# Kernel tuning notes

Hardware: AMD Instinct MI355X
Metric: run time of the kernel (lower is better)

Reference implementation:

```python
import jax, jax.numpy as jnp
import numpy as np

B, C, VC, H, W = 4, 256, 128, 64, 64


def setup_inputs() -> dict:
    key = jax.random.key(0)
    kx, kq, kk, kv = jax.random.split(key, 4)
    # Conv2d 1x1 no-bias weights are just [out_channels, in_channels] matrices.
    s = 1.0 / np.sqrt(C)
    return {
        "x": jax.random.normal(kx, (B, C, H, W), dtype=jnp.float32),
        "Wq": jax.random.uniform(kq, (VC, C), minval=-s, maxval=s, dtype=jnp.float32),
        "Wk": jax.random.uniform(kk, (VC, C), minval=-s, maxval=s, dtype=jnp.float32),
        "Wv": jax.random.uniform(kv, (VC, C), minval=-s, maxval=s, dtype=jnp.float32),
    }


def reference(x, Wq, Wk, Wv):
    # 1x1 convs == per-pixel channel GEMMs
    Q = jnp.einsum('bchw,dc->bdhw', x, Wq)  # [B, VC, H, W]
    K = jnp.einsum('bchw,dc->bdhw', x, Wk)
    V = jnp.einsum('bchw,dc->bdhw', x, Wv)
    b, d, h, w = Q.shape
    # affinity over all spatial pairs: [B, H, W, H, W]
    aff = jnp.einsum('bdij,bdkl->bijkl', Q, K).reshape(b, h, w, h * w)
    aff = jax.nn.softmax(aff, axis=3).reshape(b, h, w, h, w)
    # attention-weighted aggregation of values
    out = jnp.einsum('bijkl,bdkl->bdij', aff, V)  # [B, VC, H, W]
    return out
```

## Files before the change

### kernel.cpp

```cpp
#include <hip/hip_runtime.h>
#include <hip/hip_bf16.h>

#define B_ 4
#define C_ 256
#define D_ 128
#define N_ 4096

typedef float f32x4 __attribute__((ext_vector_type(4)));
typedef short bf16x8 __attribute__((ext_vector_type(8)));
typedef short s16x4 __attribute__((ext_vector_type(4)));
typedef unsigned short u16;
typedef unsigned int u32;

__device__ __forceinline__ u16 f2bf(float f) {
  unsigned u = __float_as_uint(f);
  u += 0x7fffu + ((u >> 16) & 1u);
  return (u16)(u >> 16);
}
__device__ __forceinline__ float bf2f(u16 v) {
  return __uint_as_float(((u32)v) << 16);
}

__global__ __launch_bounds__(256) void castw_kernel(
    const float* __restrict__ Wq, const float* __restrict__ Wk,
    const float* __restrict__ Wv, u16* __restrict__ Whi,
    u16* __restrict__ Wlo) {
  const int i = blockIdx.x * 256 + threadIdx.x;
  const int m = i >> 13;
  const int j = (i & 8191) * 4;
  const float* src = (m == 0) ? Wq : (m == 1) ? Wk : Wv;
  const float4 v = *(const float4*)(src + j);
  const float vv[4] = {v.x, v.y, v.z, v.w};
  s16x4 h, l;
#pragma unroll
  for (int k = 0; k < 4; ++k) {
    const u16 hb = f2bf(vv[k]);
    h[k] = (short)hb;
    l[k] = (short)f2bf(vv[k] - bf2f(hb));
  }
  *(s16x4*)&Whi[m * 32768 + j] = h;
  *(s16x4*)&Wlo[m * 32768 + j] = l;
}

__global__ __launch_bounds__(256, 2) void proj_kernel(
    const float* __restrict__ x, const u16* __restrict__ Whi,
    const u16* __restrict__ Wlo, u16* __restrict__ Qo, u16* __restrict__ Ko,
    u16* __restrict__ Vt) {
  __shared__ __align__(16) u16 xs_h[32 * 256];
  __shared__ __align__(16) u16 xs_l[32 * 256];

  const int n0 = blockIdx.x * 32;
  const int b = blockIdx.y;
  const int t = threadIdx.x;
  const int w = t >> 6, lane = t & 63, g = lane >> 4, c = lane & 15;

  {
    const float* xb = x + ((size_t)b * C_) * N_ + n0;
#pragma unroll
    for (int r = 0; r < 8; ++r) {
      const int id = r * 256 + t;
      const int cr = id >> 3, nq = (id & 7) * 4;
      const float4 v = *(const float4*)(xb + (size_t)cr * N_ + nq);
      const float vv[4] = {v.x, v.y, v.z, v.w};
#pragma unroll
      for (int k2 = 0; k2 < 4; ++k2) {
        const int idx2 = (nq + k2) * 256 + (cr ^ (((nq + k2) & 7) << 3));
        const u16 hb = f2bf(vv[k2]);
        xs_h[idx2] = hb;
        xs_l[idx2] = f2bf(vv[k2] - bf2f(hb));
      }
    }
  }
  __syncthreads();

  if (w < 2) {
    const size_t wo = (size_t)w * 32768;
    u16* __restrict__ O = (w == 0 ? Qo : Ko) + (size_t)b * N_ * D_;
#pragma unroll 1
    for (int dt = 0; dt < 8; ++dt) {
      bf16x8 wfh[8], wfl[8];
#pragma unroll
      for (int kc = 0; kc < 8; ++kc) {
        const size_t off = wo + (size_t)(dt * 16 + c) * 256 + kc * 32 + g * 8;
        wfh[kc] = *(const bf16x8*)&Whi[off];
        wfl[kc] = *(const bf16x8*)&Wlo[off];
      }
#pragma unroll
      for (int nt = 0; nt < 2; ++nt) {
        f32x4 a = {0.f, 0.f, 0.f, 0.f};
#pragma unroll
        for (int kc = 0; kc < 8; ++kc) {
          const int xi = (nt * 16 + c) * 256 +
                         ((kc * 32 + g * 8) ^ ((c & 7) << 3));
          const bf16x8 xh = *(const bf16x8*)&xs_h[xi];
          const bf16x8 xl = *(const bf16x8*)&xs_l[xi];
          a = __builtin_amdgcn_mfma_f32_16x16x32_bf16(xh, wfh[kc], a, 0, 0, 0);
          a = __builtin_amdgcn_mfma_f32_16x16x32_bf16(xh, wfl[kc], a, 0, 0, 0);
          a = __builtin_amdgcn_mfma_f32_16x16x32_bf16(xl, wfh[kc], a, 0, 0, 0);
        }
#pragma unroll
        for (int i = 0; i < 4; ++i)
          O[(size_t)(n0 + nt * 16 + g * 4 + i) * D_ + dt * 16 + c] = f2bf(a[i]);
      }
    }
  } else {
    const size_t wo = (size_t)2 * 32768;
    const int d0 = (w - 2) * 64;
    u16* __restrict__ O = Vt + (size_t)b * D_ * N_;
#pragma unroll 1
    for (int dt = 0; dt < 4; ++dt) {
      bf16x8 wfh[8], wfl[8];
#pragma unroll
      for (int kc = 0; kc < 8; ++kc) {
        const size_t off =
            wo + (size_t)(d0 + dt * 16 + c) * 256 + kc * 32 + g * 8;
        wfh[kc] = *(const bf16x8*)&Whi[off];
        wfl[kc] = *(const bf16x8*)&Wlo[off];
      }
#pragma unroll
      for (int nt = 0; nt < 2; ++nt) {
        f32x4 a = {0.f, 0.f, 0.f, 0.f};
#pragma unroll
        for (int kc = 0; kc < 8; ++kc) {
          const int xi = (nt * 16 + c) * 256 +
                         ((kc * 32 + g * 8) ^ ((c & 7) << 3));
          const bf16x8 xh = *(const bf16x8*)&xs_h[xi];
          const bf16x8 xl = *(const bf16x8*)&xs_l[xi];
          a = __builtin_amdgcn_mfma_f32_16x16x32_bf16(wfh[kc], xh, a, 0, 0, 0);
          a = __builtin_amdgcn_mfma_f32_16x16x32_bf16(wfl[kc], xh, a, 0, 0, 0);
          a = __builtin_amdgcn_mfma_f32_16x16x32_bf16(wfh[kc], xl, a, 0, 0, 0);
        }
#pragma unroll
        for (int i = 0; i < 4; ++i)
          O[(size_t)(d0 + dt * 16 + g * 4 + i) * N_ + n0 + nt * 16 + c] =
              f2bf(a[i]);
      }
    }
  }
}

__device__ __forceinline__ int kIdx(int row, int col) {
  return row * 128 + (col ^ ((row & 7) << 3));
}
__device__ __forceinline__ int vIdx(int d, int col) {
  return d * 64 + (col ^ ((d & 7) << 3));
}
__device__ __forceinline__ int pIdx(int q, int col) {
  return q * 64 + (col ^ ((q & 7) << 3));
}

__global__ __launch_bounds__(256, 2) void attn_kernel(
    const u16* __restrict__ Q, const u16* __restrict__ K,
    const u16* __restrict__ Vt, float* __restrict__ outp,
    float* __restrict__ mb, float* __restrict__ lb, int chunk) {
  __shared__ __align__(16) u16 lds_k[64 * 128];
  __shared__ __align__(16) u16 lds_vt[128 * 64];
  __shared__ __align__(16) u16 lds_p[4][32 * 64];

  const int b = blockIdx.y;
  const int sid = blockIdx.z;
  const int q0 = blockIdx.x * 128;
  const int k0 = sid * chunk;
  const int NT = chunk >> 6;
  const int t = threadIdx.x;
  const int w = t >> 6, lane = t & 63, g = lane >> 4, c = lane & 15;
  const int qw = q0 + w * 32;

  const u16* __restrict__ Qb = Q + (size_t)b * N_ * D_;
  const u16* __restrict__ Kb = K + (size_t)b * N_ * D_;
  const u16* __restrict__ Vb = Vt + (size_t)b * D_ * N_;

  bf16x8 qf[2][4];
#pragma unroll
  for (int qh = 0; qh < 2; ++qh)
#pragma unroll
    for (int kc = 0; kc < 4; ++kc)
      qf[qh][kc] =
          *(const bf16x8*)&Qb[(size_t)(qw + qh * 16 + c) * D_ + kc * 32 + g * 8];

  f32x4 acc[8][2];
#pragma unroll
  for (int dt = 0; dt < 8; ++dt)
#pragma unroll
    for (int qh = 0; qh < 2; ++qh) acc[dt][qh] = (f32x4){0.f, 0.f, 0.f, 0.f};
  float mrow[2] = {-3.0e38f, -3.0e38f};
  float lrow[2] = {0.f, 0.f};
  const float kE = 1.44269504f;

  bf16x8 krg[4], vrg[4];
  auto load_tile = [&](int kbase) {
#pragma unroll
    for (int i = 0; i < 4; ++i) {
      const int idx = i * 256 + t;
      krg[i] = *(const bf16x8*)&Kb[(size_t)(kbase + (idx >> 4)) * D_ + (idx & 15) * 8];
      vrg[i] = *(const bf16x8*)&Vb[(size_t)(idx >> 3) * N_ + kbase + (idx & 7) * 8];
    }
  };
  load_tile(k0);

  u16* __restrict__ pw = lds_p[w];

  for (int kt = 0; kt < NT; ++kt) {
    __syncthreads();
#pragma unroll
    for (int i = 0; i < 4; ++i) {
      const int idx = i * 256 + t;
      *(bf16x8*)&lds_k[kIdx(idx >> 4, (idx & 15) * 8)] = krg[i];
      *(bf16x8*)&lds_vt[vIdx(idx >> 3, (idx & 7) * 8)] = vrg[i];
    }
    if (kt + 1 < NT) load_tile(k0 + (kt + 1) * 64);
    __syncthreads();

    f32x4 s[4][2];
#pragma unroll
    for (int ct = 0; ct < 4; ++ct)
#pragma unroll
      for (int qh = 0; qh < 2; ++qh) s[ct][qh] = (f32x4){0.f, 0.f, 0.f, 0.f};
#pragma unroll
    for (int kc = 0; kc < 4; ++kc) {
#pragma unroll
      for (int ct = 0; ct < 4; ++ct) {
        const bf16x8 kf =
            *(const bf16x8*)&lds_k[kIdx(ct * 16 + c, kc * 32 + g * 8)];
        s[ct][0] = __builtin_amdgcn_mfma_f32_16x16x32_bf16(kf, qf[0][kc], s[ct][0], 0, 0, 0);
        s[ct][1] = __builtin_amdgcn_mfma_f32_16x16x32_bf16(kf, qf[1][kc], s[ct][1], 0, 0, 0);
      }
    }

    float pm[2];
#pragma unroll
    for (int qh = 0; qh < 2; ++qh) {
      const float m0 = fmaxf(fmaxf(s[0][qh][0], s[0][qh][1]),
                             fmaxf(s[0][qh][2], s[0][qh][3]));
      const float m1 = fmaxf(fmaxf(s[1][qh][0], s[1][qh][1]),
                             fmaxf(s[1][qh][2], s[1][qh][3]));
      const float m2 = fmaxf(fmaxf(s[2][qh][0], s[2][qh][1]),
                             fmaxf(s[2][qh][2], s[2][qh][3]));
      const float m3 = fmaxf(fmaxf(s[3][qh][0], s[3][qh][1]),
                             fmaxf(s[3][qh][2], s[3][qh][3]));
      float p = fmaxf(fmaxf(m0, m1), fmaxf(m2, m3));
      p = fmaxf(p, __shfl_xor(p, 16));
      p = fmaxf(p, __shfl_xor(p, 32));
      pm[qh] = p;
    }
    const bool need =
        __any((pm[0] > mrow[0] + 8.f) || (pm[1] > mrow[1] + 8.f));
    if (need) {
#pragma unroll
      for (int qh = 0; qh < 2; ++qh) {
        const float mnew = fmaxf(mrow[qh], pm[qh]);
        const float scl = exp2f((mrow[qh] - mnew) * kE);
        lrow[qh] *= scl;
        mrow[qh] = mnew;
#pragma unroll
        for (int dt = 0; dt < 8; ++dt) {
          acc[dt][qh][0] *= scl; acc[dt][qh][1] *= scl;
          acc[dt][qh][2] *= scl; acc[dt][qh][3] *= scl;
        }
      }
    }
#pragma unroll
    for (int qh = 0; qh < 2; ++qh) {
      float rs = 0.f;
#pragma unroll
      for (int ct = 0; ct < 4; ++ct)
#pragma unroll
        for (int i = 0; i < 4; ++i) {
          const float p = exp2f((s[ct][qh][i] - mrow[qh]) * kE);
          s[ct][qh][i] = p;
          rs += p;
        }
      rs += __shfl_xor(rs, 16);
      rs += __shfl_xor(rs, 32);
      lrow[qh] += rs;
    }

#pragma unroll
    for (int qh = 0; qh < 2; ++qh)
#pragma unroll
      for (int ct = 0; ct < 4; ++ct) {
        const int pi = pIdx(qh * 16 + c, ct * 16 + g * 4);
        s16x4 pv;
        pv[0] = (short)f2bf(s[ct][qh][0]);
        pv[1] = (short)f2bf(s[ct][qh][1]);
        pv[2] = (short)f2bf(s[ct][qh][2]);
        pv[3] = (short)f2bf(s[ct][qh][3]);
        *(s16x4*)&pw[pi] = pv;
      }
    asm volatile("" ::: "memory");

#pragma unroll
    for (int kc = 0; kc < 2; ++kc) {
      const bf16x8 pf0 = *(const bf16x8*)&pw[pIdx(c, kc * 32 + g * 8)];
      const bf16x8 pf1 = *(const bf16x8*)&pw[pIdx(16 + c, kc * 32 + g * 8)];
#pragma unroll
      for (int dt = 0; dt < 8; ++dt) {
        const bf16x8 vf =
            *(const bf16x8*)&lds_vt[vIdx(dt * 16 + c, kc * 32 + g * 8)];
        acc[dt][0] = __builtin_amdgcn_mfma_f32_16x16x32_bf16(vf, pf0, acc[dt][0], 0, 0, 0);
        acc[dt][1] = __builtin_amdgcn_mfma_f32_16x16x32_bf16(vf, pf1, acc[dt][1], 0, 0, 0);
      }
    }
  }

#pragma unroll
  for (int qh = 0; qh < 2; ++qh) {
    const int n = qw + qh * 16 + c;
    if (mb) {
      float* __restrict__ ob = outp + ((size_t)(sid * B_ + b) * D_) * N_;
#pragma unroll
      for (int dt = 0; dt < 8; ++dt)
#pragma unroll
        for (int i = 0; i < 4; ++i)
          ob[(size_t)(dt * 16 + g * 4 + i) * N_ + n] = acc[dt][qh][i];
      if (g == 0) {
        mb[(size_t)(sid * B_ + b) * N_ + n] = mrow[qh];
        lb[(size_t)(sid * B_ + b) * N_ + n] = lrow[qh];
      }
    } else {
      const float linv = 1.0f / lrow[qh];
      float* __restrict__ ob = outp + (size_t)b * D_ * N_;
#pragma unroll
      for (int dt = 0; dt < 8; ++dt)
#pragma unroll
        for (int i = 0; i < 4; ++i)
          ob[(size_t)(dt * 16 + g * 4 + i) * N_ + n] = acc[dt][qh][i] * linv;
    }
  }
}

__global__ __launch_bounds__(256) void combine_kernel(
    const float* __restrict__ op, const float* __restrict__ mbu,
    const float* __restrict__ lbu, float* __restrict__ out, int S) {
  const int idx = blockIdx.x * 256 + threadIdx.x;
  const int n0 = (idx & (N_ / 4 - 1)) * 4;
  const int bd = idx >> 10;
  const int b = bd >> 7, d = bd & (D_ - 1);
  const float kE = 1.44269504f;

  float4 msv[4], lsv[4];
  float M0 = -3e38f, M1 = -3e38f, M2 = -3e38f, M3 = -3e38f;
#pragma unroll
  for (int s = 0; s < 4; ++s)
    if (s < S) {
      msv[s] = *(const float4*)&mbu[(size_t)(s * B_ + b) * N_ + n0];
      lsv[s] = *(const float4*)&lbu[(size_t)(s * B_ + b) * N_ + n0];
      M0 = fmaxf(M0, msv[s].x); M1 = fmaxf(M1, msv[s].y);
      M2 = fmaxf(M2, msv[s].z); M3 = fmaxf(M3, msv[s].w);
    }
  float w0[4], w1[4], w2[4], w3[4];
  float d0 = 0.f, d1 = 0.f, d2 = 0.f, d3 = 0.f;
#pragma unroll
  for (int s = 0; s < 4; ++s)
    if (s < S) {
      w0[s] = exp2f((msv[s].x - M0) * kE); d0 += lsv[s].x * w0[s];
      w1[s] = exp2f((msv[s].y - M1) * kE); d1 += lsv[s].y * w1[s];
      w2[s] = exp2f((msv[s].z - M2) * kE); d2 += lsv[s].z * w2[s];
      w3[s] = exp2f((msv[s].w - M3) * kE); d3 += lsv[s].w * w3[s];
    }
  float a0 = 0.f, a1 = 0.f, a2 = 0.f, a3 = 0.f;
#pragma unroll
  for (int s = 0; s < 4; ++s)
    if (s < S) {
      const float4 o =
          *(const float4*)&op[((size_t)(s * B_ + b) * D_ + d) * N_ + n0];
      a0 += w0[s] * o.x; a1 += w1[s] * o.y;
      a2 += w2[s] * o.z; a3 += w3[s] * o.w;
    }
  float4 r = {a0 / d0, a1 / d1, a2 / d2, a3 / d3};
  *(float4*)&out[((size_t)b * D_ + d) * N_ + n0] = r;
}

extern "C" void kernel_launch(void* const* d_in, const int* in_sizes, int n_in,
                              void* d_out, int out_size, void* d_ws, size_t ws_size,
                              hipStream_t stream) {
  const float* x  = (const float*)d_in[0];
  const float* Wq = (const float*)d_in[1];
  const float* Wk = (const float*)d_in[2];
  const float* Wv = (const float*)d_in[3];
  float* out = (float*)d_out;

  u16* whi  = (u16*)d_ws;
  u16* wlo  = whi + (size_t)3 * 128 * 256;
  u16* q_ws = wlo + (size_t)3 * 128 * 256;
  u16* k_ws = q_ws + (size_t)B_ * N_ * D_;
  u16* v_ws = k_ws + (size_t)B_ * N_ * D_;

  castw_kernel<<<96, 256, 0, stream>>>(Wq, Wk, Wv, whi, wlo);
  proj_kernel<<<dim3(N_ / 32, B_), 256, 0, stream>>>(x, whi, wlo, q_ws, k_ws,
                                                     v_ws);

  const size_t baseB =
      ((size_t)6 * 128 * 256 + (size_t)3 * B_ * N_ * D_) * 2;
  int S = 0;
  for (int cand = 4; cand >= 1; cand >>= 1) {
    const size_t need = baseB + (size_t)cand * ((size_t)B_ * D_ * N_ * 4 +
                                                (size_t)2 * B_ * N_ * 4);
    if (ws_size >= need) { S = cand; break; }
  }
  if (S > 0) {
    float* op = (float*)((char*)d_ws + baseB);
    float* mbuf = op + (size_t)S * B_ * D_ * N_;
    float* lbuf = mbuf + (size_t)S * B_ * N_;
    attn_kernel<<<dim3(N_ / 128, B_, S), 256, 0, stream>>>(
        q_ws, k_ws, v_ws, op, mbuf, lbuf, N_ / S);
    combine_kernel<<<(B_ * D_ * N_ / 4) / 256, 256, 0, stream>>>(op, mbuf,
                                                                 lbuf, out, S);
  } else {
    attn_kernel<<<dim3(N_ / 128, B_, 1), 256, 0, stream>>>(
        q_ws, k_ws, v_ws, out, nullptr, nullptr, N_);
  }
}
```

Before: 103.5 us.

## Keep P in registers via lane shuffles, bf16 partials, split-K up to 8

Drops the per-wave LDS staging of the softmax probabilities. P is packed to bf16 in registers and exchanged across lanes with xor-32 shuffles, and the V tile is stored into LDS with a matching column permutation so the PV MFMA operands line up. Partial attention outputs are written as bf16 instead of fp32, which halves the split-K workspace and lets the split count rise to 8. Occupancy is raised to 3 blocks per SIMD, and s_setprio is placed around the MFMA loops. The bf16 partials lose precision, and the higher split count adds combine work.

```diff
diff --git a/kernel.cpp b/kernel.cpp
--- a/kernel.cpp
+++ b/kernel.cpp
@@ -19,6 +19,9 @@
 }
 __device__ __forceinline__ float bf2f(u16 v) {
   return __uint_as_float(((u32)v) << 16);
+}
+__device__ __forceinline__ u32 pack2(float a, float b) {
+  return (u32)f2bf(a) | ((u32)f2bf(b) << 16);
 }
 
 __global__ __launch_bounds__(256) void castw_kernel(
@@ -145,17 +148,19 @@
 __device__ __forceinline__ int vIdx(int d, int col) {
   return d * 64 + (col ^ ((d & 7) << 3));
 }
-__device__ __forceinline__ int pIdx(int q, int col) {
-  return q * 64 + (col ^ ((q & 7) << 3));
-}
-
-__global__ __launch_bounds__(256, 2) void attn_kernel(
+__device__ __forceinline__ int kprm(int q) {
+  const int ct = q >> 2, qq = q & 3;
+  return ((ct >> 1) << 5) +
+         (((qq >> 1) == (ct & 1)) ? (qq << 3) : (((qq ^ 2) << 3) + 4));
+}
+
+__global__ __launch_bounds__(256, 3) void attn_kernel(
     const u16* __restrict__ Q, const u16* __restrict__ K,
-    const u16* __restrict__ Vt, float* __restrict__ outp,
-    float* __restrict__ mb, float* __restrict__ lb, int chunk) {
+    const u16* __restrict__ Vt, u16* __restrict__ op,
+    float* __restrict__ mb, float* __restrict__ lb,
+    float* __restrict__ outf, int chunk) {
   __shared__ __align__(16) u16 lds_k[64 * 128];
   __shared__ __align__(16) u16 lds_vt[128 * 64];
-  __shared__ __align__(16) u16 lds_p[4][32 * 64];
 
   const int b = blockIdx.y;
   const int sid = blockIdx.z;
@@ -165,6 +170,7 @@
   const int t = threadIdx.x;
   const int w = t >> 6, lane = t & 63, g = lane >> 4, c = lane & 15;
   const int qw = q0 + w * 32;
+  const bool ghi = (g & 2) != 0;
 
   const u16* __restrict__ Qb = Q + (size_t)b * N_ * D_;
   const u16* __restrict__ Kb = K + (size_t)b * N_ * D_;
@@ -198,15 +204,18 @@
   };
   load_tile(k0);
 
-  u16* __restrict__ pw = lds_p[w];
-
   for (int kt = 0; kt < NT; ++kt) {
     __syncthreads();
 #pragma unroll
     for (int i = 0; i < 4; ++i) {
       const int idx = i * 256 + t;
       *(bf16x8*)&lds_k[kIdx(idx >> 4, (idx & 15) * 8)] = krg[i];
-      *(bf16x8*)&lds_vt[vIdx(idx >> 3, (idx & 7) * 8)] = vrg[i];
+      const int d = idx >> 3, rc = idx & 7;
+      s16x4 lo, hi;
+      lo[0] = vrg[i][0]; lo[1] = vrg[i][1]; lo[2] = vrg[i][2]; lo[3] = vrg[i][3];
+      hi[0] = vrg[i][4]; hi[1] = vrg[i][5]; hi[2] = vrg[i][6]; hi[3] = vrg[i][7];
+      *(s16x4*)&lds_vt[vIdx(d, kprm(rc * 2))] = lo;
+      *(s16x4*)&lds_vt[vIdx(d, kprm(rc * 2 + 1))] = hi;
     }
     if (kt + 1 < NT) load_tile(k0 + (kt + 1) * 64);
     __syncthreads();
@@ -216,6 +225,7 @@
     for (int ct = 0; ct < 4; ++ct)
 #pragma unroll
       for (int qh = 0; qh < 2; ++qh) s[ct][qh] = (f32x4){0.f, 0.f, 0.f, 0.f};
+    __builtin_amdgcn_s_setprio(1);
 #pragma unroll
     for (int kc = 0; kc < 4; ++kc) {
 #pragma unroll
@@ -226,6 +236,7 @@
         s[ct][1] = __builtin_amdgcn_mfma_f32_16x16x32_bf16(kf, qf[1][kc], s[ct][1], 0, 0, 0);
       }
     }
+    __builtin_amdgcn_s_setprio(0);
 
     float pm[2];
 #pragma unroll
@@ -275,31 +286,38 @@
       lrow[qh] += rs;
     }
 
-#pragma unroll
-    for (int qh = 0; qh < 2; ++qh)
-#pragma unroll
-      for (int ct = 0; ct < 4; ++ct) {
-        const int pi = pIdx(qh * 16 + c, ct * 16 + g * 4);
-        s16x4 pv;
-        pv[0] = (short)f2bf(s[ct][qh][0]);
-        pv[1] = (short)f2bf(s[ct][qh][1]);
-        pv[2] = (short)f2bf(s[ct][qh][2]);
-        pv[3] = (short)f2bf(s[ct][qh][3]);
-        *(s16x4*)&pw[pi] = pv;
-      }
-    asm volatile("" ::: "memory");
-
+    u32 pfw[2][2][4];
 #pragma unroll
     for (int kc = 0; kc < 2; ++kc) {
-      const bf16x8 pf0 = *(const bf16x8*)&pw[pIdx(c, kc * 32 + g * 8)];
-      const bf16x8 pf1 = *(const bf16x8*)&pw[pIdx(16 + c, kc * 32 + g * 8)];
+#pragma unroll
+      for (int qh = 0; qh < 2; ++qh) {
+        const u32 lo0 = pack2(s[kc * 2][qh][0], s[kc * 2][qh][1]);
+        const u32 lo1 = pack2(s[kc * 2][qh][2], s[kc * 2][qh][3]);
+        const u32 hi0 = pack2(s[kc * 2 + 1][qh][0], s[kc * 2 + 1][qh][1]);
+        const u32 hi1 = pack2(s[kc * 2 + 1][qh][2], s[kc * 2 + 1][qh][3]);
+        pfw[kc][qh][0] = ghi ? hi0 : lo0;
+        pfw[kc][qh][1] = ghi ? hi1 : lo1;
+        const u32 s0 = ghi ? lo0 : hi0;
+        const u32 s1 = ghi ? lo1 : hi1;
+        pfw[kc][qh][2] = (u32)__shfl_xor((int)s0, 32);
+        pfw[kc][qh][3] = (u32)__shfl_xor((int)s1, 32);
+      }
+    }
+
+#pragma unroll
+    for (int kc = 0; kc < 2; ++kc) {
+      union { u32 w[4]; bf16x8 v; } u0, u1;
+#pragma unroll
+      for (int j = 0; j < 4; ++j) { u0.w[j] = pfw[kc][0][j]; u1.w[j] = pfw[kc][1][j]; }
+      __builtin_amdgcn_s_setprio(1);
 #pragma unroll
       for (int dt = 0; dt < 8; ++dt) {
         const bf16x8 vf =
             *(const bf16x8*)&lds_vt[vIdx(dt * 16 + c, kc * 32 + g * 8)];
-        acc[dt][0] = __builtin_amdgcn_mfma_f32_16x16x32_bf16(vf, pf0, acc[dt][0], 0, 0, 0);
-        acc[dt][1] = __builtin_amdgcn_mfma_f32_16x16x32_bf16(vf, pf1, acc[dt][1], 0, 0, 0);
-      }
+        acc[dt][0] = __builtin_amdgcn_mfma_f32_16x16x32_bf16(vf, u0.v, acc[dt][0], 0, 0, 0);
+        acc[dt][1] = __builtin_amdgcn_mfma_f32_16x16x32_bf16(vf, u1.v, acc[dt][1], 0, 0, 0);
+      }
+      __builtin_amdgcn_s_setprio(0);
     }
   }
 
@@ -307,19 +325,19 @@
   for (int qh = 0; qh < 2; ++qh) {
     const int n = qw + qh * 16 + c;
     if (mb) {
-      float* __restrict__ ob = outp + ((size_t)(sid * B_ + b) * D_) * N_;
+      u16* __restrict__ ob = op + ((size_t)(sid * B_ + b) * D_) * N_;
 #pragma unroll
       for (int dt = 0; dt < 8; ++dt)
 #pragma unroll
         for (int i = 0; i < 4; ++i)
-          ob[(size_t)(dt * 16 + g * 4 + i) * N_ + n] = acc[dt][qh][i];
+          ob[(size_t)(dt * 16 + g * 4 + i) * N_ + n] = f2bf(acc[dt][qh][i]);
       if (g == 0) {
         mb[(size_t)(sid * B_ + b) * N_ + n] = mrow[qh];
         lb[(size_t)(sid * B_ + b) * N_ + n] = lrow[qh];
       }
     } else {
       const float linv = 1.0f / lrow[qh];
-      float* __restrict__ ob = outp + (size_t)b * D_ * N_;
+      float* __restrict__ ob = outf + (size_t)b * D_ * N_;
 #pragma unroll
       for (int dt = 0; dt < 8; ++dt)
 #pragma unroll
@@ -330,7 +348,7 @@
 }
 
 __global__ __launch_bounds__(256) void combine_kernel(
-    const float* __restrict__ op, const float* __restrict__ mbu,
+    const u16* __restrict__ op, const float* __restrict__ mbu,
     const float* __restrict__ lbu, float* __restrict__ out, int S) {
   const int idx = blockIdx.x * 256 + threadIdx.x;
   const int n0 = (idx & (N_ / 4 - 1)) * 4;
@@ -338,34 +356,31 @@
   const int b = bd >> 7, d = bd & (D_ - 1);
   const float kE = 1.44269504f;
 
-  float4 msv[4], lsv[4];
+  float4 msv[8], lsv[8];
   float M0 = -3e38f, M1 = -3e38f, M2 = -3e38f, M3 = -3e38f;
 #pragma unroll
-  for (int s = 0; s < 4; ++s)
+  for (int s = 0; s < 8; ++s)
     if (s < S) {
       msv[s] = *(const float4*)&mbu[(size_t)(s * B_ + b) * N_ + n0];
       lsv[s] = *(const float4*)&lbu[(size_t)(s * B_ + b) * N_ + n0];
       M0 = fmaxf(M0, msv[s].x); M1 = fmaxf(M1, msv[s].y);
       M2 = fmaxf(M2, msv[s].z); M3 = fmaxf(M3, msv[s].w);
     }
-  float w0[4], w1[4], w2[4], w3[4];
   float d0 = 0.f, d1 = 0.f, d2 = 0.f, d3 = 0.f;
-#pragma unroll
-  for (int s = 0; s < 4; ++s)
+  float a0 = 0.f, a1 = 0.f, a2 = 0.f, a3 = 0.f;
+#pragma unroll
+  for (int s = 0; s < 8; ++s)
     if (s < S) {
-      w0[s] = exp2f((msv[s].x - M0) * kE); d0 += lsv[s].x * w0[s];
-      w1[s] = exp2f((msv[s].y - M1) * kE); d1 += lsv[s].y * w1[s];
-      w2[s] = exp2f((msv[s].z - M2) * kE); d2 += lsv[s].z * w2[s];
-      w3[s] = exp2f((msv[s].w - M3) * kE); d3 += lsv[s].w * w3[s];
-    }
-  float a0 = 0.f, a1 = 0.f, a2 = 0.f, a3 = 0.f;
-#pragma unroll
-  for (int s = 0; s < 4; ++s)
-    if (s < S) {
-      const float4 o =
-          *(const float4*)&op[((size_t)(s * B_ + b) * D_ + d) * N_ + n0];
-      a0 += w0[s] * o.x; a1 += w1[s] * o.y;
-      a2 += w2[s] * o.z; a3 += w3[s] * o.w;
+      const float w0 = exp2f((msv[s].x - M0) * kE);
+      const float w1 = exp2f((msv[s].y - M1) * kE);
+      const float w2 = exp2f((msv[s].z - M2) * kE);
+      const float w3 = exp2f((msv[s].w - M3) * kE);
+      d0 += lsv[s].x * w0; d1 += lsv[s].y * w1;
+      d2 += lsv[s].z * w2; d3 += lsv[s].w * w3;
+      const s16x4 o =
+          *(const s16x4*)&op[((size_t)(s * B_ + b) * D_ + d) * N_ + n0];
+      a0 += w0 * bf2f((u16)o[0]); a1 += w1 * bf2f((u16)o[1]);
+      a2 += w2 * bf2f((u16)o[2]); a3 += w3 * bf2f((u16)o[3]);
     }
   float4 r = {a0 / d0, a1 / d1, a2 / d2, a3 / d3};
   *(float4*)&out[((size_t)b * D_ + d) * N_ + n0] = r;
@@ -393,21 +408,21 @@
   const size_t baseB =
       ((size_t)6 * 128 * 256 + (size_t)3 * B_ * N_ * D_) * 2;
   int S = 0;
-  for (int cand = 4; cand >= 1; cand >>= 1) {
-    const size_t need = baseB + (size_t)cand * ((size_t)B_ * D_ * N_ * 4 +
+  for (int cand = 8; cand >= 1; cand >>= 1) {
+    const size_t need = baseB + (size_t)cand * ((size_t)B_ * D_ * N_ * 2 +
                                                 (size_t)2 * B_ * N_ * 4);
     if (ws_size >= need) { S = cand; break; }
   }
   if (S > 0) {
-    float* op = (float*)((char*)d_ws + baseB);
-    float* mbuf = op + (size_t)S * B_ * D_ * N_;
+    u16* opb = (u16*)((char*)d_ws + baseB);
+    float* mbuf = (float*)(opb + (size_t)S * B_ * D_ * N_);
     float* lbuf = mbuf + (size_t)S * B_ * N_;
     attn_kernel<<<dim3(N_ / 128, B_, S), 256, 0, stream>>>(
-        q_ws, k_ws, v_ws, op, mbuf, lbuf, N_ / S);
-    combine_kernel<<<(B_ * D_ * N_ / 4) / 256, 256, 0, stream>>>(op, mbuf,
+        q_ws, k_ws, v_ws, opb, mbuf, lbuf, nullptr, N_ / S);
+    combine_kernel<<<(B_ * D_ * N_ / 4) / 256, 256, 0, stream>>>(opb, mbuf,
                                                                  lbuf, out, S);
   } else {
     attn_kernel<<<dim3(N_ / 128, B_, 1), 256, 0, stream>>>(
-        q_ws, k_ws, v_ws, out, nullptr, nullptr, N_);
-  }
-}
+        q_ws, k_ws, v_ws, nullptr, nullptr, nullptr, out, N_);
+  }
+}
```

Result: slower. 217.4 us (+110.2%).
